# Kernel optimization log

Hardware: AMD Instinct MI355X
Metric: run time of the kernel (lower is better)

## Reference

```python
import jax, jax.numpy as jnp
import numpy as np

B, N, DH = 256, 32, 128      # batch, n_agents, per-agent hidden
E = 496                       # n_edges (fully connected over 32 agents)
DIM_IN = 2 * DH               # 256, MLP input (concat of two agent states)
DIM_HID = 256
A = 12                        # dim_act
R = 4                         # payoff_rank
DIM_OUT = 2 * R * A           # 96


def setup_inputs() -> dict:
    key = jax.random.key(0)
    ks = jax.random.split(key, 7)
    hidden_states_n = jax.random.normal(ks[0], (B, N, DH), dtype=jnp.float32)
    edges_from = jax.random.randint(ks[1], (E,), 0, N, dtype=jnp.int32).astype(jnp.int64)
    edges_to = jax.random.randint(ks[2], (E,), 0, N, dtype=jnp.int32).astype(jnp.int64)
    # torch.nn.Linear params: W [out, in], b [out]
    W1 = jax.random.normal(ks[3], (DIM_HID, DIM_IN), dtype=jnp.float32) * (1.0 / np.sqrt(DIM_IN))
    b1 = jnp.zeros((DIM_HID,), dtype=jnp.float32)
    W2 = jax.random.normal(ks[4], (DIM_OUT, DIM_HID), dtype=jnp.float32) * (1.0 / np.sqrt(DIM_HID))
    b2 = jnp.zeros((DIM_OUT,), dtype=jnp.float32)
    return {"hidden_states_n": hidden_states_n, "W1": W1, "b1": b1, "W2": W2,
            "b2": b2, "edges_from": edges_from, "edges_to": edges_to}


def reference(hidden_states_n, W1, b1, W2, b2, edges_from, edges_to):
    hf = hidden_states_n[:, edges_from]                     # [B, E, DH]
    ht = hidden_states_n[:, edges_to]                       # [B, E, DH]
    # stack of (from||to, to||from): [2, B, E, 2*DH]
    inp = jnp.stack([jnp.concatenate([hf, ht], axis=-1),
                     jnp.concatenate([ht, hf], axis=-1)], axis=0)
    h = jax.nn.relu(inp @ W1.T + b1)                        # [2, B, E, DIM_HID]
    p = h @ W2.T + b2                                       # [2, B, E, 2*R*A]
    p = p.reshape(2, B, E, R, 2, A)
    # low-rank outer product per rank, summed over ranks: [2, B, E, A, A]
    payoffs = jnp.einsum('sberi,sberj->sbeij', p[..., 0, :], p[..., 1, :])
    # second copy is transposed, then mean over the two directions
    return 0.5 * (payoffs[0] + jnp.swapaxes(payoffs[1], -1, -2))  # [B, E, A, A]
```

## Files before the change

### kernel.cpp

```cpp
#include <hip/hip_runtime.h>

typedef unsigned int uint;
typedef unsigned short ushort_t;

typedef __attribute__((ext_vector_type(8))) short bf16x8;
typedef __attribute__((ext_vector_type(4))) float f32x4;

#define E_CNT 496

__device__ __forceinline__ ushort_t f32_to_bf16_rn(float x) {
    uint u = __float_as_uint(x);
    u = (u + 0x7fffu + ((u >> 16) & 1u)) >> 16;
    return (ushort_t)u;
}

__global__ __launch_bounds__(256) void prep_kernel(const int* __restrict__ sf, const int* __restrict__ st,
                                                   const float* __restrict__ W1,
                                                   int* __restrict__ ef, int* __restrict__ et,
                                                   float* __restrict__ W1T) {
    const int tid = threadIdx.x;
    if (blockIdx.x == 0) {
        bool f64 = true, t64 = true;
        #pragma unroll
        for (int i = 0; i < 16; ++i) {
            if (sf[2 * i + 1] != 0) f64 = false;
            if (st[2 * i + 1] != 0) t64 = false;
        }
        for (int j = tid; j < E_CNT; j += 256) {
            ef[j] = f64 ? sf[2 * j] : sf[j];
            et[j] = t64 ? st[2 * j] : st[j];
        }
        return;
    }
    __shared__ float tile[64][65];
    const int t = blockIdx.x - 1;
    const int tr = t >> 2;
    const int tc = t & 3;
    const int tx = tid & 63;
    const int ty4 = tid >> 6;
    #pragma unroll
    for (int rr = 0; rr < 16; ++rr) {
        int row = rr * 4 + ty4;
        tile[row][tx] = W1[(tr * 64 + row) * 256 + tc * 64 + tx];
    }
    __syncthreads();
    #pragma unroll
    for (int rr = 0; rr < 16; ++rr) {
        int row = rr * 4 + ty4;
        W1T[(tc * 64 + row) * 256 + tr * 64 + tx] = tile[tx][row];
    }
}

__global__ __launch_bounds__(256) void x_kernel(const float* __restrict__ hidden,
                                                const float* __restrict__ W1T,
                                                const float* __restrict__ b1,
                                                ushort_t* __restrict__ X1,
                                                ushort_t* __restrict__ X2) {
    const int h = threadIdx.x;
    const int row0 = blockIdx.x * 16;
    const float* __restrict__ hb = hidden + row0 * 128;
    const float* __restrict__ w1ta = W1T + h;
    const float* __restrict__ w1tb = W1T + 128 * 256 + h;

    float acc1[16], acc2[16];
    #pragma unroll
    for (int r = 0; r < 16; ++r) { acc1[r] = 0.f; acc2[r] = 0.f; }

    #pragma unroll 4
    for (int d = 0; d < 128; ++d) {
        float wa = w1ta[d * 256];
        float wb = w1tb[d * 256];
        #pragma unroll
        for (int r = 0; r < 16; ++r) {
            float hv = hb[r * 128 + d];
            acc1[r] = fmaf(wa, hv, acc1[r]);
            acc2[r] = fmaf(wb, hv, acc2[r]);
        }
    }
    float bh = 0.5f * b1[h];
    #pragma unroll
    for (int r = 0; r < 16; ++r) {
        X1[(row0 + r) * 256 + h] = f32_to_bf16_rn(acc1[r] + bh);
        X2[(row0 + r) * 256 + h] = f32_to_bf16_rn(acc2[r] + bh);
    }
}

#define PAIR_STRIDE 100
#define R_OFF 800
#define WAVE_PF 1600

__global__ __launch_bounds__(512) void gemm_payoff_kernel(
    const ushort_t* __restrict__ X1, const ushort_t* __restrict__ X2,
    const int* __restrict__ ef, const int* __restrict__ et,
    const float* __restrict__ W2, const float* __restrict__ b2,
    float* __restrict__ out) {

    __shared__ __align__(16) unsigned char smem[51200];
    ushort_t* w2s = (ushort_t*)smem;
    float* pf = (float*)smem;

    const int tid = threadIdx.x;

    #pragma unroll
    for (int j = 0; j < 12; ++j) {
        int idx4 = tid + j * 512;
        int n = idx4 >> 6;
        int k = (idx4 & 63) << 2;
        float4 v = *(const float4*)&W2[n * 256 + k];
        ushort_t* dst = &w2s[n * 264 + k];
        dst[0] = f32_to_bf16_rn(v.x);
        dst[1] = f32_to_bf16_rn(v.y);
        dst[2] = f32_to_bf16_rn(v.z);
        dst[3] = f32_to_bf16_rn(v.w);
    }

    const int ln = tid & 63;
    const int waveId = tid >> 6;
    const int quad = ln >> 4;
    const int l16 = ln & 15;
    const int pl = l16 & 7;
    const int s = l16 >> 3;

    const int pairBase = blockIdx.x * 64 + waveId * 8;
    const int pair = pairBase + pl;
    const int b = pair / E_CNT;
    const int e = pair - b * E_CNT;
    const int f = ef[e];
    const int t = et[e];
    const int n1 = s ? t : f;
    const int n2 = s ? f : t;
    const ushort_t* px1 = X1 + ((b * 32 + n1) * 256 + quad * 8);
    const ushort_t* px2 = X2 + ((b * 32 + n2) * 256 + quad * 8);

    float b2v[6];
    #pragma unroll
    for (int tt = 0; tt < 6; ++tt) b2v[tt] = b2[tt * 16 + l16];

    f32x4 acc[6];
    #pragma unroll
    for (int tt = 0; tt < 6; ++tt) acc[tt] = (f32x4){0.f, 0.f, 0.f, 0.f};

    __syncthreads();

    #pragma unroll
    for (int kk = 0; kk < 8; ++kk) {
        uint4 a1 = *(const uint4*)(px1 + kk * 32);
        uint4 a2 = *(const uint4*)(px2 + kk * 32);
        uint ua[4] = {a1.x, a1.y, a1.z, a1.w};
        uint ub[4] = {a2.x, a2.y, a2.z, a2.w};
        union { uint u[4]; bf16x8 v; } af;
        #pragma unroll
        for (int w = 0; w < 4; ++w) {
            float lo = __uint_as_float(ua[w] << 16) + __uint_as_float(ub[w] << 16);
            float hi = __uint_as_float(ua[w] & 0xffff0000u) + __uint_as_float(ub[w] & 0xffff0000u);
            lo = fmaxf(lo, 0.f);
            hi = fmaxf(hi, 0.f);
            af.u[w] = (__float_as_uint(lo) >> 16) | (__float_as_uint(hi) & 0xffff0000u);
        }
        #pragma unroll
        for (int tt = 0; tt < 6; ++tt) {
            const int nrow = tt * 16 + l16;
            bf16x8 bf = *(const bf16x8*)&w2s[nrow * 264 + kk * 32 + quad * 8];
            acc[tt] = __builtin_amdgcn_mfma_f32_16x16x32_bf16(af.v, bf, acc[tt], 0, 0, 0);
        }
    }

    __syncthreads();

    float* wbase = pf + waveId * WAVE_PF;
    #pragma unroll
    for (int tt = 0; tt < 6; ++tt) {
        const int n = tt * 16 + l16;
        const int rr = n / 24;
        const int rem = n - rr * 24;
        const int c01 = (rem >= 12) ? 1 : 0;
        const int a = rem - c01 * 12;
        #pragma unroll
        for (int r = 0; r < 4; ++r) {
            const int row = quad * 4 + r;
            const int s_ = row >> 3;
            const int pl_ = row & 7;
            const int k8 = (s_ ? 4 : 0) + rr;
            const int toL = (c01 == s_) ? 1 : 0;
            float val = acc[tt][r] + b2v[tt];
            wbase[(toL ? 0 : R_OFF) + pl_ * PAIR_STRIDE + a * 8 + k8] = val;
        }
    }

    __syncthreads();

    #pragma unroll
    for (int it = 0; it < 2; ++it) {
        int task = it * 64 + ln;
        if (task < 96) {
            int pp = task / 12;
            int i = task - pp * 12;
            const float* Lp = wbase + pp * PAIR_STRIDE + i * 8;
            float4 l0 = *(const float4*)&Lp[0];
            float4 l1 = *(const float4*)&Lp[4];
            float od[12];
            #pragma unroll
            for (int jj = 0; jj < 12; ++jj) {
                const float* Rp = wbase + R_OFF + pp * PAIR_STRIDE + jj * 8;
                float4 r0 = *(const float4*)&Rp[0];
                float4 r1 = *(const float4*)&Rp[4];
                float d = l0.x * r0.x + l0.y * r0.y + l0.z * r0.z + l0.w * r0.w
                        + l1.x * r1.x + l1.y * r1.y + l1.z * r1.z + l1.w * r1.w;
                od[jj] = 0.5f * d;
            }
            int outBase = (pairBase + pp) * 144 + i * 12;
            *(float4*)&out[outBase + 0] = make_float4(od[0], od[1], od[2], od[3]);
            *(float4*)&out[outBase + 4] = make_float4(od[4], od[5], od[6], od[7]);
            *(float4*)&out[outBase + 8] = make_float4(od[8], od[9], od[10], od[11]);
        }
    }
}

extern "C" void kernel_launch(void* const* d_in, const int* in_sizes, int n_in,
                              void* d_out, int out_size, void* d_ws, size_t ws_size,
                              hipStream_t stream) {
    const float* hidden = (const float*)d_in[0];
    const float* W1 = (const float*)d_in[1];
    const float* b1 = (const float*)d_in[2];
    const float* W2 = (const float*)d_in[3];
    const float* b2 = (const float*)d_in[4];
    const int* e_f = (const int*)d_in[5];
    const int* e_t = (const int*)d_in[6];
    float* out = (float*)d_out;

    char* ws = (char*)d_ws;
    int* ef = (int*)ws;
    int* et = (int*)(ws + 2048);
    float* W1T = (float*)(ws + 8192);
    ushort_t* X1 = (ushort_t*)(ws + 270336);
    ushort_t* X2 = (ushort_t*)(ws + 270336 + 4 * 1024 * 1024);

    prep_kernel<<<17, 256, 0, stream>>>(e_f, e_t, W1, ef, et, W1T);
    x_kernel<<<512, 256, 0, stream>>>(hidden, W1T, b1, X1, X2);
    gemm_payoff_kernel<<<1984, 512, 0, stream>>>(X1, X2, ef, et, W2, b2, out);
}
```

Measured before the change: 158.8 us.

## Use MFMA for node projection, pre-pack bf16 weights, double pairs per wave

The per-node W1 projection is rewritten from a scalar FP32 FMA loop into bf16 MFMA tiles. W1 is pre-converted by the prep kernel into an XOR-swizzled bf16 image that is staged in LDS. W2 is likewise pre-converted to a bf16 padded image, so each payoff block copies it with vector loads instead of converting per block. The payoff kernel now processes two 8-pair M-tiles per wave, which halves the grid and amortizes the W2 LDS load and B-fragment reads. In exchange, hidden states are rounded to bf16 before the first GEMM, and register pressure in the payoff kernel rises.

```diff
diff --git a/kernel.cpp b/kernel.cpp
--- a/kernel.cpp
+++ b/kernel.cpp
@@ -13,13 +13,47 @@
     u = (u + 0x7fffu + ((u >> 16) & 1u)) >> 16;
     return (ushort_t)u;
 }
-
-__global__ __launch_bounds__(256) void prep_kernel(const int* __restrict__ sf, const int* __restrict__ st,
-                                                   const float* __restrict__ W1,
-                                                   int* __restrict__ ef, int* __restrict__ et,
-                                                   float* __restrict__ W1T) {
+__device__ __forceinline__ uint pack2_bf16(float lo, float hi) {
+    return (uint)f32_to_bf16_rn(lo) | ((uint)f32_to_bf16_rn(hi) << 16);
+}
+
+__global__ __launch_bounds__(256) void prep_kernel(
+    const int* __restrict__ sf, const int* __restrict__ st,
+    const float* __restrict__ W1, const float* __restrict__ W2,
+    int* __restrict__ ef, int* __restrict__ et,
+    ushort_t* __restrict__ w1img, ushort_t* __restrict__ w2img) {
     const int tid = threadIdx.x;
-    if (blockIdx.x == 0) {
+    const int blk = blockIdx.x;
+    if (blk < 32) {
+        int gid = blk * 256 + tid;
+        int half = gid >> 12;
+        int rem = gid & 4095;
+        int h = rem >> 4;
+        int c = rem & 15;
+        const float* src = W1 + h * 256 + half * 128 + c * 8;
+        float4 v0 = *(const float4*)src;
+        float4 v1 = *(const float4*)(src + 4);
+        uint4 o;
+        o.x = pack2_bf16(v0.x, v0.y);
+        o.y = pack2_bf16(v0.z, v0.w);
+        o.z = pack2_bf16(v1.x, v1.y);
+        o.w = pack2_bf16(v1.z, v1.w);
+        int dst = half * 32768 + h * 128 + ((c ^ (h & 7)) << 3);
+        *(uint4*)(w1img + dst) = o;
+    } else if (blk < 44) {
+        int gid = (blk - 32) * 256 + tid;
+        int n = gid >> 5;
+        int c = gid & 31;
+        const float* src = W2 + n * 256 + c * 8;
+        float4 v0 = *(const float4*)src;
+        float4 v1 = *(const float4*)(src + 4);
+        uint4 o;
+        o.x = pack2_bf16(v0.x, v0.y);
+        o.y = pack2_bf16(v0.z, v0.w);
+        o.z = pack2_bf16(v1.x, v1.y);
+        o.w = pack2_bf16(v1.z, v1.w);
+        *(uint4*)(w2img + n * 264 + c * 8) = o;
+    } else {
         bool f64 = true, t64 = true;
         #pragma unroll
         for (int i = 0; i < 16; ++i) {
@@ -30,58 +64,61 @@
             ef[j] = f64 ? sf[2 * j] : sf[j];
             et[j] = t64 ? st[2 * j] : st[j];
         }
-        return;
-    }
-    __shared__ float tile[64][65];
-    const int t = blockIdx.x - 1;
-    const int tr = t >> 2;
-    const int tc = t & 3;
-    const int tx = tid & 63;
-    const int ty4 = tid >> 6;
-    #pragma unroll
-    for (int rr = 0; rr < 16; ++rr) {
-        int row = rr * 4 + ty4;
-        tile[row][tx] = W1[(tr * 64 + row) * 256 + tc * 64 + tx];
+    }
+}
+
+__global__ __launch_bounds__(256) void x_kernel(
+    const float* __restrict__ hidden, const ushort_t* __restrict__ w1img,
+    const float* __restrict__ b1, ushort_t* __restrict__ Xout) {
+    __shared__ __align__(16) ushort_t w1s[256 * 128];
+
+    const int tid = threadIdx.x;
+    const int half = blockIdx.x & 1;
+    const int mblk = blockIdx.x >> 1;
+
+    {
+        const uint4* gsrc = (const uint4*)(w1img + half * 32768);
+        uint4* ldst = (uint4*)w1s;
+        #pragma unroll
+        for (int j = 0; j < 16; ++j) ldst[tid + j * 256] = gsrc[tid + j * 256];
+    }
+
+    const int ln = tid & 63;
+    const int waveId = tid >> 6;
+    const int quad = ln >> 4;
+    const int l16 = ln & 15;
+    const int row0 = mblk * 64 + waveId * 16;
+
+    union { uint u[4]; bf16x8 v; } af[4];
+    const float* arow = hidden + (row0 + l16) * 128 + quad * 8;
+    #pragma unroll
+    for (int kk = 0; kk < 4; ++kk) {
+        float4 v0 = *(const float4*)(arow + kk * 32);
+        float4 v1 = *(const float4*)(arow + kk * 32 + 4);
+        af[kk].u[0] = pack2_bf16(v0.x, v0.y);
+        af[kk].u[1] = pack2_bf16(v0.z, v0.w);
+        af[kk].u[2] = pack2_bf16(v1.x, v1.y);
+        af[kk].u[3] = pack2_bf16(v1.z, v1.w);
     }
     __syncthreads();
-    #pragma unroll
-    for (int rr = 0; rr < 16; ++rr) {
-        int row = rr * 4 + ty4;
-        W1T[(tc * 64 + row) * 256 + tr * 64 + tx] = tile[tx][row];
-    }
-}
-
-__global__ __launch_bounds__(256) void x_kernel(const float* __restrict__ hidden,
-                                                const float* __restrict__ W1T,
-                                                const float* __restrict__ b1,
-                                                ushort_t* __restrict__ X1,
-                                                ushort_t* __restrict__ X2) {
-    const int h = threadIdx.x;
-    const int row0 = blockIdx.x * 16;
-    const float* __restrict__ hb = hidden + row0 * 128;
-    const float* __restrict__ w1ta = W1T + h;
-    const float* __restrict__ w1tb = W1T + 128 * 256 + h;
-
-    float acc1[16], acc2[16];
-    #pragma unroll
-    for (int r = 0; r < 16; ++r) { acc1[r] = 0.f; acc2[r] = 0.f; }
-
-    #pragma unroll 4
-    for (int d = 0; d < 128; ++d) {
-        float wa = w1ta[d * 256];
-        float wb = w1tb[d * 256];
-        #pragma unroll
-        for (int r = 0; r < 16; ++r) {
-            float hv = hb[r * 128 + d];
-            acc1[r] = fmaf(wa, hv, acc1[r]);
-            acc2[r] = fmaf(wb, hv, acc2[r]);
-        }
-    }
-    float bh = 0.5f * b1[h];
-    #pragma unroll
-    for (int r = 0; r < 16; ++r) {
-        X1[(row0 + r) * 256 + h] = f32_to_bf16_rn(acc1[r] + bh);
-        X2[(row0 + r) * 256 + h] = f32_to_bf16_rn(acc2[r] + bh);
+
+    ushort_t* xbase = Xout + half * (8192 * 256);
+    #pragma unroll
+    for (int nt = 0; nt < 16; ++nt) {
+        const int h = nt * 16 + l16;
+        f32x4 acc = (f32x4){0.f, 0.f, 0.f, 0.f};
+        #pragma unroll
+        for (int kk = 0; kk < 4; ++kk) {
+            const int c_log = kk * 4 + quad;
+            bf16x8 bf = *(const bf16x8*)&w1s[h * 128 + ((c_log ^ (h & 7)) << 3)];
+            acc = __builtin_amdgcn_mfma_f32_16x16x32_bf16(af[kk].v, bf, acc, 0, 0, 0);
+        }
+        const float bh = 0.5f * b1[h];
+        #pragma unroll
+        for (int r = 0; r < 4; ++r) {
+            const int row = row0 + quad * 4 + r;
+            xbase[row * 256 + h] = f32_to_bf16_rn(acc[r] + bh);
+        }
     }
 }
 
@@ -89,10 +126,10 @@
 #define R_OFF 800
 #define WAVE_PF 1600
 
-__global__ __launch_bounds__(512) void gemm_payoff_kernel(
+__global__ __launch_bounds__(512, 4) void gemm_payoff_kernel(
     const ushort_t* __restrict__ X1, const ushort_t* __restrict__ X2,
     const int* __restrict__ ef, const int* __restrict__ et,
-    const float* __restrict__ W2, const float* __restrict__ b2,
+    const ushort_t* __restrict__ w2img, const float* __restrict__ b2,
     float* __restrict__ out) {
 
     __shared__ __align__(16) unsigned char smem[51200];
@@ -101,17 +138,14 @@
 
     const int tid = threadIdx.x;
 
-    #pragma unroll
-    for (int j = 0; j < 12; ++j) {
-        int idx4 = tid + j * 512;
-        int n = idx4 >> 6;
-        int k = (idx4 & 63) << 2;
-        float4 v = *(const float4*)&W2[n * 256 + k];
-        ushort_t* dst = &w2s[n * 264 + k];
-        dst[0] = f32_to_bf16_rn(v.x);
-        dst[1] = f32_to_bf16_rn(v.y);
-        dst[2] = f32_to_bf16_rn(v.z);
-        dst[3] = f32_to_bf16_rn(v.w);
+    {
+        const uint4* src = (const uint4*)w2img;
+        uint4* dst = (uint4*)smem;
+        #pragma unroll
+        for (int j = 0; j < 7; ++j) {
+            int idx = tid + j * 512;
+            if (idx < 3168) dst[idx] = src[idx];
+        }
     }
 
     const int ln = tid & 63;
@@ -121,97 +155,108 @@
     const int pl = l16 & 7;
     const int s = l16 >> 3;
 
-    const int pairBase = blockIdx.x * 64 + waveId * 8;
-    const int pair = pairBase + pl;
-    const int b = pair / E_CNT;
-    const int e = pair - b * E_CNT;
-    const int f = ef[e];
-    const int t = et[e];
-    const int n1 = s ? t : f;
-    const int n2 = s ? f : t;
-    const ushort_t* px1 = X1 + ((b * 32 + n1) * 256 + quad * 8);
-    const ushort_t* px2 = X2 + ((b * 32 + n2) * 256 + quad * 8);
+    const int pairBase = blockIdx.x * 128 + waveId * 16;
+    const ushort_t* px1[2];
+    const ushort_t* px2[2];
+    #pragma unroll
+    for (int mt = 0; mt < 2; ++mt) {
+        int pair = pairBase + mt * 8 + pl;
+        int b = pair / E_CNT;
+        int e = pair - b * E_CNT;
+        int f = ef[e];
+        int t = et[e];
+        int n1 = s ? t : f;
+        int n2 = s ? f : t;
+        px1[mt] = X1 + ((b * 32 + n1) * 256 + quad * 8);
+        px2[mt] = X2 + ((b * 32 + n2) * 256 + quad * 8);
+    }
 
     float b2v[6];
     #pragma unroll
     for (int tt = 0; tt < 6; ++tt) b2v[tt] = b2[tt * 16 + l16];
 
-    f32x4 acc[6];
-    #pragma unroll
-    for (int tt = 0; tt < 6; ++tt) acc[tt] = (f32x4){0.f, 0.f, 0.f, 0.f};
+    f32x4 acc[2][6];
+    #pragma unroll
+    for (int mt = 0; mt < 2; ++mt)
+        #pragma unroll
+        for (int tt = 0; tt < 6; ++tt) acc[mt][tt] = (f32x4){0.f, 0.f, 0.f, 0.f};
 
     __syncthreads();
 
     #pragma unroll
     for (int kk = 0; kk < 8; ++kk) {
-        uint4 a1 = *(const uint4*)(px1 + kk * 32);
-        uint4 a2 = *(const uint4*)(px2 + kk * 32);
-        uint ua[4] = {a1.x, a1.y, a1.z, a1.w};
-        uint ub[4] = {a2.x, a2.y, a2.z, a2.w};
-        union { uint u[4]; bf16x8 v; } af;
-        #pragma unroll
-        for (int w = 0; w < 4; ++w) {
-            float lo = __uint_as_float(ua[w] << 16) + __uint_as_float(ub[w] << 16);
-            float hi = __uint_as_float(ua[w] & 0xffff0000u) + __uint_as_float(ub[w] & 0xffff0000u);
-            lo = fmaxf(lo, 0.f);
-            hi = fmaxf(hi, 0.f);
-            af.u[w] = (__float_as_uint(lo) >> 16) | (__float_as_uint(hi) & 0xffff0000u);
+        union { uint u[4]; bf16x8 v; } af[2];
+        #pragma unroll
+        for (int mt = 0; mt < 2; ++mt) {
+            uint4 a1 = *(const uint4*)(px1[mt] + kk * 32);
+            uint4 a2 = *(const uint4*)(px2[mt] + kk * 32);
+            uint ua[4] = {a1.x, a1.y, a1.z, a1.w};
+            uint ub[4] = {a2.x, a2.y, a2.z, a2.w};
+            #pragma unroll
+            for (int w = 0; w < 4; ++w) {
+                float lo = __uint_as_float(ua[w] << 16) + __uint_as_float(ub[w] << 16);
+                float hi = __uint_as_float(ua[w] & 0xffff0000u) + __uint_as_float(ub[w] & 0xffff0000u);
+                lo = fmaxf(lo, 0.f);
+                hi = fmaxf(hi, 0.f);
+                af[mt].u[w] = (__float_as_uint(lo) >> 16) | (__float_as_uint(hi) & 0xffff0000u);
+            }
         }
         #pragma unroll
         for (int tt = 0; tt < 6; ++tt) {
-            const int nrow = tt * 16 + l16;
-            bf16x8 bf = *(const bf16x8*)&w2s[nrow * 264 + kk * 32 + quad * 8];
-            acc[tt] = __builtin_amdgcn_mfma_f32_16x16x32_bf16(af.v, bf, acc[tt], 0, 0, 0);
-        }
-    }
-
-    __syncthreads();
+            bf16x8 bf = *(const bf16x8*)&w2s[(tt * 16 + l16) * 264 + kk * 32 + quad * 8];
+            acc[0][tt] = __builtin_amdgcn_mfma_f32_16x16x32_bf16(af[0].v, bf, acc[0][tt], 0, 0, 0);
+            acc[1][tt] = __builtin_amdgcn_mfma_f32_16x16x32_bf16(af[1].v, bf, acc[1][tt], 0, 0, 0);
+        }
+    }
 
     float* wbase = pf + waveId * WAVE_PF;
     #pragma unroll
-    for (int tt = 0; tt < 6; ++tt) {
-        const int n = tt * 16 + l16;
-        const int rr = n / 24;
-        const int rem = n - rr * 24;
-        const int c01 = (rem >= 12) ? 1 : 0;
-        const int a = rem - c01 * 12;
-        #pragma unroll
-        for (int r = 0; r < 4; ++r) {
-            const int row = quad * 4 + r;
-            const int s_ = row >> 3;
-            const int pl_ = row & 7;
-            const int k8 = (s_ ? 4 : 0) + rr;
-            const int toL = (c01 == s_) ? 1 : 0;
-            float val = acc[tt][r] + b2v[tt];
-            wbase[(toL ? 0 : R_OFF) + pl_ * PAIR_STRIDE + a * 8 + k8] = val;
-        }
-    }
-
-    __syncthreads();
-
-    #pragma unroll
-    for (int it = 0; it < 2; ++it) {
-        int task = it * 64 + ln;
-        if (task < 96) {
-            int pp = task / 12;
-            int i = task - pp * 12;
-            const float* Lp = wbase + pp * PAIR_STRIDE + i * 8;
-            float4 l0 = *(const float4*)&Lp[0];
-            float4 l1 = *(const float4*)&Lp[4];
-            float od[12];
+    for (int mt = 0; mt < 2; ++mt) {
+        __syncthreads();
+
+        #pragma unroll
+        for (int tt = 0; tt < 6; ++tt) {
+            const int n = tt * 16 + l16;
+            const int rr = n / 24;
+            const int rem = n - rr * 24;
+            const int c01 = (rem >= 12) ? 1 : 0;
+            const int a = rem - c01 * 12;
             #pragma unroll
-            for (int jj = 0; jj < 12; ++jj) {
-                const float* Rp = wbase + R_OFF + pp * PAIR_STRIDE + jj * 8;
-                float4 r0 = *(const float4*)&Rp[0];
-                float4 r1 = *(const float4*)&Rp[4];
-                float d = l0.x * r0.x + l0.y * r0.y + l0.z * r0.z + l0.w * r0.w
-                        + l1.x * r1.x + l1.y * r1.y + l1.z * r1.z + l1.w * r1.w;
-                od[jj] = 0.5f * d;
+            for (int r = 0; r < 4; ++r) {
+                const int row = quad * 4 + r;
+                const int s_ = row >> 3;
+                const int pl_ = row & 7;
+                const int k8 = (s_ ? 4 : 0) + rr;
+                const int toL = (c01 == s_) ? 1 : 0;
+                wbase[(toL ? 0 : R_OFF) + pl_ * PAIR_STRIDE + a * 8 + k8] = acc[mt][tt][r] + b2v[tt];
             }
-            int outBase = (pairBase + pp) * 144 + i * 12;
-            *(float4*)&out[outBase + 0] = make_float4(od[0], od[1], od[2], od[3]);
-            *(float4*)&out[outBase + 4] = make_float4(od[4], od[5], od[6], od[7]);
-            *(float4*)&out[outBase + 8] = make_float4(od[8], od[9], od[10], od[11]);
+        }
+        __syncthreads();
+
+        #pragma unroll
+        for (int it = 0; it < 2; ++it) {
+            int task = it * 64 + ln;
+            if (task < 96) {
+                int pp = task / 12;
+                int i = task - pp * 12;
+                const float* Lp = wbase + pp * PAIR_STRIDE + i * 8;
+                float4 l0 = *(const float4*)&Lp[0];
+                float4 l1 = *(const float4*)&Lp[4];
+                float od[12];
+                #pragma unroll
+                for (int jj = 0; jj < 12; ++jj) {
+                    const float* Rp = wbase + R_OFF + pp * PAIR_STRIDE + jj * 8;
+                    float4 r0 = *(const float4*)&Rp[0];
+                    float4 r1 = *(const float4*)&Rp[4];
+                    float d = l0.x * r0.x + l0.y * r0.y + l0.z * r0.z + l0.w * r0.w
+                            + l1.x * r1.x + l1.y * r1.y + l1.z * r1.z + l1.w * r1.w;
+                    od[jj] = 0.5f * d;
+                }
+                int outBase = (pairBase + mt * 8 + pp) * 144 + i * 12;
+                *(float4*)&out[outBase + 0] = make_float4(od[0], od[1], od[2], od[3]);
+                *(float4*)&out[outBase + 4] = make_float4(od[4], od[5], od[6], od[7]);
+                *(float4*)&out[outBase + 8] = make_float4(od[8], od[9], od[10], od[11]);
+            }
         }
     }
 }
@@ -230,12 +275,12 @@
 
     char* ws = (char*)d_ws;
     int* ef = (int*)ws;
-    int* et = (int*)(ws + 2048);
-    float* W1T = (float*)(ws + 8192);
-    ushort_t* X1 = (ushort_t*)(ws + 270336);
-    ushort_t* X2 = (ushort_t*)(ws + 270336 + 4 * 1024 * 1024);
-
-    prep_kernel<<<17, 256, 0, stream>>>(e_f, e_t, W1, ef, et, W1T);
-    x_kernel<<<512, 256, 0, stream>>>(hidden, W1T, b1, X1, X2);
-    gemm_payoff_kernel<<<1984, 512, 0, stream>>>(X1, X2, ef, et, W2, b2, out);
-}
+    int* et = (int*)(ws + 4096);
+    ushort_t* w1img = (ushort_t*)(ws + 8192);
+    ushort_t* w2img = (ushort_t*)(ws + 139264);
+    ushort_t* X = (ushort_t*)(ws + 190464);
+
+    prep_kernel<<<45, 256, 0, stream>>>(e_f, e_t, W1, W2, ef, et, w1img, w2img);
+    x_kernel<<<256, 256, 0, stream>>>(hidden, w1img, b1, X);
+    gemm_payoff_kernel<<<992, 512, 0, stream>>>(X, X + 8192 * 256, ef, et, w2img, b2, out);
+}
```

After: 146.9 us. 7.5% less time.
